# Optimization experiments

Hardware: AMD Instinct MI355X
Metric: run time of the kernel (lower is better)

## Reference

```python
import jax, jax.numpy as jnp
import numpy as np

N_GENE, N_CELL, N_GOTEM = 20000, 50000, 8000
D = 128
E_GC, E_GT = 600000, 200000


def _gconv(x_src, W, b, src, dst, n_src, n_dst):
    """DGL GraphConv with norm='both', bias, ReLU activation.
    out = relu(D_in^{-1/2} * scatter_sum_dst( (D_out^{-1/2} x_src) @ W ) + b)
    Degrees clamped to min 1, computed per edge type (as DGL does)."""
    ones = jnp.ones(src.shape[0], x_src.dtype)
    deg_out = jnp.clip(jax.ops.segment_sum(ones, src, num_segments=n_src), 1.0)
    deg_in = jnp.clip(jax.ops.segment_sum(ones, dst, num_segments=n_dst), 1.0)
    h = (x_src * (deg_out ** -0.5)[:, None]) @ W          # [n_src, d_out]
    agg = jax.ops.segment_sum(h[src], dst, num_segments=n_dst)  # gather + scatter-sum
    return jax.nn.relu(agg * (deg_in ** -0.5)[:, None] + b)


def setup_inputs() -> dict:
    key = jax.random.key(0)
    ks = iter(jax.random.split(key, 64))
    s = 1.0 / np.sqrt(D)
    inp = {
        "x_gene": jax.random.normal(next(ks), (N_GENE, D), jnp.float32),
        "x_cell": jax.random.normal(next(ks), (N_CELL, D), jnp.float32),
        "x_gotem": jax.random.normal(next(ks), (N_GOTEM, D), jnp.float32),
    }
    for name in ["W_eg_c2g", "W_eg_t2g", "W_eg_g2c", "W_et_g2t",
                 "W1_g2c", "W1_c2g", "W1_g2t", "W1_t2g",
                 "W2_g2c", "W2_c2g", "W2_g2t", "W2_t2g",
                 "W3_g2c", "Wd_cell"]:
        inp[name] = jax.random.normal(next(ks), (D, D), jnp.float32) * s
        inp[name.replace("W", "b", 1)] = jnp.zeros((D,), jnp.float32)
    inp["eg2c_src"] = jax.random.randint(next(ks), (E_GC,), 0, N_GENE, jnp.int32)
    inp["eg2c_dst"] = jax.random.randint(next(ks), (E_GC,), 0, N_CELL, jnp.int32)
    inp["ec2g_src"] = jax.random.randint(next(ks), (E_GC,), 0, N_CELL, jnp.int32)
    inp["ec2g_dst"] = jax.random.randint(next(ks), (E_GC,), 0, N_GENE, jnp.int32)
    inp["eg2t_src"] = jax.random.randint(next(ks), (E_GT,), 0, N_GENE, jnp.int32)
    inp["eg2t_dst"] = jax.random.randint(next(ks), (E_GT,), 0, N_GOTEM, jnp.int32)
    inp["et2g_src"] = jax.random.randint(next(ks), (E_GT,), 0, N_GOTEM, jnp.int32)
    inp["et2g_dst"] = jax.random.randint(next(ks), (E_GT,), 0, N_GENE, jnp.int32)
    return inp


def reference(x_gene, x_cell, x_gotem,
              W_eg_c2g, b_eg_c2g, W_eg_t2g, b_eg_t2g, W_eg_g2c, b_eg_g2c,
              W_et_g2t, b_et_g2t,
              W1_g2c, b1_g2c, W1_c2g, b1_c2g, W1_g2t, b1_g2t, W1_t2g, b1_t2g,
              W2_g2c, b2_g2c, W2_c2g, b2_c2g, W2_g2t, b2_g2t, W2_t2g, b2_t2g,
              W3_g2c, b3_g2c, Wd_cell, bd_cell,
              eg2c_src, eg2c_dst, ec2g_src, ec2g_dst,
              eg2t_src, eg2t_dst, et2g_src, et2g_dst):
    ng, nc, nt = x_gene.shape[0], x_cell.shape[0], x_gotem.shape[0]
    # embedding_gene: HeteroGraphConv(sum) -> gene gets cell2gene + gotem2gene, cell gets gene2cell
    h0_gene = (_gconv(x_cell, W_eg_c2g, b_eg_c2g, ec2g_src, ec2g_dst, nc, ng)
               + _gconv(x_gotem, W_eg_t2g, b_eg_t2g, et2g_src, et2g_dst, nt, ng))
    h0_cell = _gconv(x_gene, W_eg_g2c, b_eg_g2c, eg2c_src, eg2c_dst, ng, nc)
    g = jax.nn.relu(h0_gene)   # extra relu in forward (idempotent but faithful)
    c = jax.nn.relu(h0_cell)
    # embedding_gotem uses the UPDATED gene features
    t = _gconv(g, W_et_g2t, b_et_g2t, eg2t_src, eg2t_dst, ng, nt)
    # conv1
    g1 = (_gconv(c, W1_c2g, b1_c2g, ec2g_src, ec2g_dst, nc, ng)
          + _gconv(t, W1_t2g, b1_t2g, et2g_src, et2g_dst, nt, ng))
    c1 = _gconv(g, W1_g2c, b1_g2c, eg2c_src, eg2c_dst, ng, nc)
    t1 = _gconv(g, W1_g2t, b1_g2t, eg2t_src, eg2t_dst, ng, nt)
    # conv2
    g2 = (_gconv(c1, W2_c2g, b2_c2g, ec2g_src, ec2g_dst, nc, ng)
          + _gconv(t1, W2_t2g, b2_t2g, et2g_src, et2g_dst, nt, ng))
    c2 = _gconv(g1, W2_g2c, b2_g2c, eg2c_src, eg2c_dst, ng, nc)
    del t1
    # conv3: only the 'cell' output feeds the returned value
    c3 = _gconv(g2, W3_g2c, b3_g2c, eg2c_src, eg2c_dst, ng, nc)
    del c2
    # HeteroLinear on 'cell' (no activation)
    return c3 @ Wd_cell + bd_cell
```

## Files before the change

### kernel.cpp

```cpp
#include <hip/hip_runtime.h>
#include <hip/hip_fp16.h>

#define NG 20000
#define NC 50000
#define NT 8000
#define EGC 600000
#define EGT 200000
#define CHUNK 25000


struct HSeg { const int* idx; int* rep; int* pos; int ne, nb, bpr, nranges, nd; };
struct HTab { HSeg s[12]; };

static __global__ __launch_bounds__(1024)
void hist_lds_kernel(HTab tab) {
    __shared__ int h[12800];
    int b = blockIdx.x, sidx = 0;
    for (;;) {
        int nbl = tab.s[sidx].nb * tab.s[sidx].nranges;
        if (b < nbl) break;
        b -= nbl; ++sidx;
    }
    const HSeg g = tab.s[sidx];
    const int row = b % g.nb, range = b / g.nb;
    const int lo = range * g.bpr;
    const int hi = min(lo + g.bpr, g.nd);
    const int nbins = hi - lo;
    for (int i = threadIdx.x; i < nbins; i += 1024) h[i] = 0;
    __syncthreads();
    const int e0 = row * CHUNK;
    const int e1 = min(e0 + CHUNK, g.ne);
    if (g.pos) {
        for (int i = e0 + (int)threadIdx.x; i < e1; i += 1024) {
            int d = g.idx[i];
            if (d >= lo && d < hi) {
                int p = atomicAdd(&h[d - lo], 1);
                g.pos[i] = p;
            }
        }
    } else {
        for (int i = e0 + (int)threadIdx.x; i < e1; i += 1024) {
            int d = g.idx[i];
            if (d >= lo && d < hi) atomicAdd(&h[d - lo], 1);
        }
    }
    __syncthreads();
    int* rp = g.rep + (size_t)row * g.nd + lo;
    for (int i = threadIdx.x; i < nbins; i += 1024) rp[i] = h[i];
}


struct SPSeg { int* repd; const int* reps; float* so; float* si; int* ci_tot; int ns, nd, nb, len; };

static __device__ void sp_body(const SPSeg& s, int i) {
    if (i < s.ns) {
        int c = 0;
        for (int r = 0; r < s.nb; ++r) c += s.reps[(size_t)r * s.ns + i];
        if (c < 1) c = 1;
        s.so[i] = 1.0f / sqrtf((float)c);
    }
    if (i < s.nd) {
        int run = 0;
        for (int r = 0; r < s.nb; ++r) {
            int* p = s.repd + (size_t)r * s.nd + i;
            int t = *p; *p = run; run += t;
        }
        s.ci_tot[i] = run;
        int c = run < 1 ? 1 : run;
        s.si[i] = 1.0f / sqrtf((float)c);
    }
}

static __global__ __launch_bounds__(256)
void spscales4_kernel(SPSeg a, SPSeg b, SPSeg c, SPSeg d) {
    int i = blockIdx.x * 256 + threadIdx.x;
    if (i < a.len) { sp_body(a, i); return; }
    i -= a.len;
    if (i < b.len) { sp_body(b, i); return; }
    i -= b.len;
    if (i < c.len) { sp_body(c, i); return; }
    i -= c.len;
    if (i < d.len) { sp_body(d, i); }
}


static __global__ __launch_bounds__(256)
void xconv_kernel(const float* __restrict__ x, const float* __restrict__ so,
                  float2* __restrict__ out) {
    int i = blockIdx.x * 256 + threadIdx.x;
    if (i >= NC * 32) return;
    int row = i >> 5;
    float s = so[row];
    float4 v = reinterpret_cast<const float4*>(x)[i];
    float2 pk;
    *reinterpret_cast<__half2*>(&pk.x) = __floats2half2_rn(v.x * s, v.y * s);
    *reinterpret_cast<__half2*>(&pk.y) = __floats2half2_rn(v.z * s, v.w * s);
    out[i] = pk;
}


static __device__ void scan_body(const int* __restrict__ cnt, int* __restrict__ off, int n) {
    __shared__ int wsum[16];
    __shared__ int carry_s, total_s;
    const int t = threadIdx.x;
    const int lane = t & 63, wid = t >> 6;
    if (t == 0) carry_s = 0;
    __syncthreads();
    for (int base = 0; base < n; base += 8192) {
        int i0 = base + t * 8;
        int v[8];
        if (i0 + 8 <= n) {
            int4 a = *reinterpret_cast<const int4*>(cnt + i0);
            int4 b = *reinterpret_cast<const int4*>(cnt + i0 + 4);
            v[0]=a.x; v[1]=a.y; v[2]=a.z; v[3]=a.w; v[4]=b.x; v[5]=b.y; v[6]=b.z; v[7]=b.w;
        } else {
#pragma unroll
            for (int k = 0; k < 8; ++k) v[k] = (i0 + k < n) ? cnt[i0 + k] : 0;
        }
        int tsum = 0;
#pragma unroll
        for (int k = 0; k < 8; ++k) tsum += v[k];
        int x = tsum;
#pragma unroll
        for (int d = 1; d < 64; d <<= 1) {
            int y = __shfl_up(x, d, 64);
            if (lane >= d) x += y;
        }
        if (lane == 63) wsum[wid] = x;
        __syncthreads();
        if (wid == 0) {
            int w = (lane < 16) ? wsum[lane] : 0;
            int xx = w;
#pragma unroll
            for (int d = 1; d < 16; d <<= 1) {
                int y = __shfl_up(xx, d, 64);
                if (lane >= d) xx += y;
            }
            if (lane < 16) wsum[lane] = xx - w;
            if (lane == 15) total_s = xx;
        }
        __syncthreads();
        int run = carry_s + wsum[wid] + (x - tsum);
        if (i0 + 8 <= n) {
            int o[8];
#pragma unroll
            for (int k = 0; k < 8; ++k) { o[k] = run; run += v[k]; }
            *reinterpret_cast<int4*>(off + i0)     = make_int4(o[0], o[1], o[2], o[3]);
            *reinterpret_cast<int4*>(off + i0 + 4) = make_int4(o[4], o[5], o[6], o[7]);
        } else {
#pragma unroll
            for (int k = 0; k < 8; ++k) if (i0 + k < n) { off[i0 + k] = run; run += v[k]; }
        }
        __syncthreads();
        if (t == 0) carry_s += total_s;
        __syncthreads();
    }
    if (t == 0) off[n] = carry_s;
}

static __global__ __launch_bounds__(1024)
void scan4_kernel(const int* c0, int* o0, int n0,
                  const int* c1, int* o1, int n1,
                  const int* c2, int* o2, int n2,
                  const int* c3, int* o3, int n3) {
    if (blockIdx.x == 0) scan_body(c0, o0, n0);
    else if (blockIdx.x == 1) scan_body(c1, o1, n1);
    else if (blockIdx.x == 2) scan_body(c2, o2, n2);
    else scan_body(c3, o3, n3);
}


struct SSeg { const int* srce; const int* dste; const int* pos; const int* rep; const int* off; int* eid; int ne, nd; };

static __device__ void scatter_body(const SSeg& s, int i) {
    int row = i / CHUNK;
    int d = s.dste[i];
    s.eid[s.off[d] + s.rep[(size_t)row * s.nd + d] + s.pos[i]] = s.srce[i];
}

static __global__ __launch_bounds__(256)
void scatter4_kernel(SSeg a, SSeg b, SSeg c, SSeg d) {
    int i = blockIdx.x * 256 + threadIdx.x;
    if (i < a.ne) { scatter_body(a, i); return; }
    i -= a.ne;
    if (i < b.ne) { scatter_body(b, i); return; }
    i -= b.ne;
    if (i < c.ne) { scatter_body(c, i); return; }
    i -= c.ne;
    if (i < d.ne) { scatter_body(d, i); }
}


template<int RELU, int RH, int WH>
static __global__ __launch_bounds__(256)
void gemm_kernel(const void* __restrict__ Xv, const float* __restrict__ rs,
                 const float* __restrict__ W, const float* __restrict__ bias,
                 void* __restrict__ outv, int n) {
    __shared__ float xs[32][128];
    const int r0 = blockIdx.x * 32;
    const int t = threadIdx.x;
    for (int i = t; i < 1024; i += 256) {
        int r = i >> 5;
        int c4 = i & 31;
        int row = r0 + r;
        float4 v = make_float4(0.f, 0.f, 0.f, 0.f);
        if (row < n) {
            if (RH) {
                float2 pk = reinterpret_cast<const float2*>(Xv)[row * 32 + c4];
                float2 lo = __half22float2(*reinterpret_cast<__half2*>(&pk.x));
                float2 hi = __half22float2(*reinterpret_cast<__half2*>(&pk.y));
                v = make_float4(lo.x, lo.y, hi.x, hi.y);
            } else {
                v = reinterpret_cast<const float4*>(Xv)[row * 32 + c4];
            }
            if (rs) { float s = rs[row]; v.x *= s; v.y *= s; v.z *= s; v.w *= s; }
        }
        reinterpret_cast<float4*>(&xs[r][0])[c4] = v;
    }
    __syncthreads();
    const int tx = t & 31, ty = t >> 5;
    const int c0 = tx << 2;
    float acc[4][4] = {};
    const float* wp = W + c0;
    for (int k = 0; k < 128; k += 4) {
        float4 w0 = *reinterpret_cast<const float4*>(wp + (k + 0) * 128);
        float4 w1 = *reinterpret_cast<const float4*>(wp + (k + 1) * 128);
        float4 w2 = *reinterpret_cast<const float4*>(wp + (k + 2) * 128);
        float4 w3 = *reinterpret_cast<const float4*>(wp + (k + 3) * 128);
#pragma unroll
        for (int i = 0; i < 4; ++i) {
            float4 xv = *reinterpret_cast<const float4*>(&xs[ty * 4 + i][k]);
            acc[i][0] += xv.x * w0.x; acc[i][1] += xv.x * w0.y; acc[i][2] += xv.x * w0.z; acc[i][3] += xv.x * w0.w;
            acc[i][0] += xv.y * w1.x; acc[i][1] += xv.y * w1.y; acc[i][2] += xv.y * w1.z; acc[i][3] += xv.y * w1.w;
            acc[i][0] += xv.z * w2.x; acc[i][1] += xv.z * w2.y; acc[i][2] += xv.z * w2.z; acc[i][3] += xv.z * w2.w;
            acc[i][0] += xv.w * w3.x; acc[i][1] += xv.w * w3.y; acc[i][2] += xv.w * w3.z; acc[i][3] += xv.w * w3.w;
        }
    }
    float4 bv = make_float4(0.f, 0.f, 0.f, 0.f);
    if (bias) bv = reinterpret_cast<const float4*>(bias)[tx];
#pragma unroll
    for (int i = 0; i < 4; ++i) {
        int row = r0 + ty * 4 + i;
        if (row < n) {
            float4 o;
            o.x = acc[i][0] + bv.x; o.y = acc[i][1] + bv.y;
            o.z = acc[i][2] + bv.z; o.w = acc[i][3] + bv.w;
            if (RELU) {
                o.x = fmaxf(o.x, 0.f); o.y = fmaxf(o.y, 0.f);
                o.z = fmaxf(o.z, 0.f); o.w = fmaxf(o.w, 0.f);
            }
            if (WH) {
                float2 pk;
                *reinterpret_cast<__half2*>(&pk.x) = __floats2half2_rn(o.x, o.y);
                *reinterpret_cast<__half2*>(&pk.y) = __floats2half2_rn(o.z, o.w);
                reinterpret_cast<float2*>(outv)[row * 32 + tx] = pk;
            } else {
                reinterpret_cast<float4*>(outv)[row * 32 + tx] = o;
            }
        }
    }
}


template<int MODE, int OUTH>
static __global__ __launch_bounds__(256)
void agg_kernel(const __half2* __restrict__ h2, const float* __restrict__ pre,
                const int* __restrict__ off, const int* __restrict__ eid,
                const float* __restrict__ si, const float* __restrict__ bias,
                const float* __restrict__ post,
                void* __restrict__ outv, int n_dst) {
    int row = blockIdx.x * 4 + (threadIdx.x >> 6);
    if (row >= n_dst) return;
    int lane = threadIdx.x & 63;
    int e0 = off[row], e1 = off[row + 1];
    float ax = 0.f, ay = 0.f;
    int j = e0;
    for (; j + 8 <= e1; j += 8) {
        int s[8];
#pragma unroll
        for (int k = 0; k < 8; ++k) s[k] = eid[j + k];
        float2 f[8];
#pragma unroll
        for (int k = 0; k < 8; ++k) f[k] = __half22float2(h2[(size_t)s[k] * 64 + lane]);
        if (pre) {
#pragma unroll
            for (int k = 0; k < 8; ++k) { float p = pre[s[k]]; ax += f[k].x * p; ay += f[k].y * p; }
        } else {
#pragma unroll
            for (int k = 0; k < 8; ++k) { ax += f[k].x; ay += f[k].y; }
        }
    }
    for (; j < e1; ++j) {
        int s = eid[j];
        float2 f = __half22float2(h2[(size_t)s * 64 + lane]);
        float p = pre ? pre[s] : 1.0f;
        ax += f.x * p; ay += f.y * p;
    }
    int oidx = row * 64 + lane;
    if (MODE == 0) {
        reinterpret_cast<float2*>(outv)[oidx] = make_float2(ax, ay);
    } else {
        float s = si[row];
        float2 b = reinterpret_cast<const float2*>(bias)[lane];
        float ox = fmaxf(ax * s + b.x, 0.f);
        float oy = fmaxf(ay * s + b.y, 0.f);
        if (MODE == 1 && post) { float pm = post[row]; ox *= pm; oy *= pm; }
        if (OUTH) {
            __half2* o = reinterpret_cast<__half2*>(outv) + oidx;
            if (MODE == 2) { float2 cur = __half22float2(*o); ox += cur.x; oy += cur.y; }
            *o = __floats2half2_rn(ox, oy);
        } else {
            float2* o = reinterpret_cast<float2*>(outv) + oidx;
            if (MODE == 2) { float2 cur = *o; ox += cur.x; oy += cur.y; }
            *o = make_float2(ox, oy);
        }
    }
}


extern "C" void kernel_launch(void* const* d_in, const int* in_sizes, int n_in,
                              void* d_out, int out_size, void* d_ws, size_t ws_size,
                              hipStream_t stream) {
    const float* x_cell   = (const float*)d_in[1];
    const float* x_gotem  = (const float*)d_in[2];
    const float* W_eg_c2g = (const float*)d_in[3];  const float* b_eg_c2g = (const float*)d_in[4];
    const float* W_eg_t2g = (const float*)d_in[5];  const float* b_eg_t2g = (const float*)d_in[6];
    const float* W1_g2c   = (const float*)d_in[11]; const float* b1_g2c   = (const float*)d_in[12];
    const float* W1_g2t   = (const float*)d_in[15]; const float* b1_g2t   = (const float*)d_in[16];
    const float* W2_c2g   = (const float*)d_in[21]; const float* b2_c2g   = (const float*)d_in[22];
    const float* W2_t2g   = (const float*)d_in[25]; const float* b2_t2g   = (const float*)d_in[26];
    const float* W3_g2c   = (const float*)d_in[27]; const float* b3_g2c   = (const float*)d_in[28];
    const float* Wd_cell  = (const float*)d_in[29]; const float* bd_cell  = (const float*)d_in[30];
    const int* eg2c_src = (const int*)d_in[31]; const int* eg2c_dst = (const int*)d_in[32];
    const int* ec2g_src = (const int*)d_in[33]; const int* ec2g_dst = (const int*)d_in[34];
    const int* eg2t_src = (const int*)d_in[35]; const int* eg2t_dst = (const int*)d_in[36];
    const int* et2g_src = (const int*)d_in[37]; const int* et2g_dst = (const int*)d_in[38];

    char* p = (char*)d_ws;
    auto alloc = [&](size_t bytes) { char* r = p; p += (bytes + 255) & ~(size_t)255; return r; };
    float* h_buf = (float*)alloc((size_t)NC * 128 * 4);
    void*  g_buf = (void*)alloc((size_t)NG * 128 * 2);
    void*  c_buf = (void*)alloc((size_t)NC * 128 * 4);
    float* t_buf = (float*)alloc((size_t)NT * 128 * 4);
    void*  xch   = (void*)alloc((size_t)NC * 128 * 2);
    int* off_gc = (int*)alloc((NG + 1) * 4);  int* eid_gc = (int*)alloc((size_t)EGC * 4);
    int* off_gt = (int*)alloc((NG + 1) * 4);  int* eid_gt = (int*)alloc((size_t)EGT * 4);
    int* off_c  = (int*)alloc((NC + 1) * 4);  int* eid_c  = (int*)alloc((size_t)EGC * 4);
    int* off_t  = (int*)alloc((NT + 1) * 4);  int* eid_t  = (int*)alloc((size_t)EGT * 4);
    float* so_ec2g = (float*)alloc(NC * 4);
    float* so_et2g = (float*)alloc(NT * 4);
    float* so_eg2c = (float*)alloc(NG * 4);
    float* so_eg2t = (float*)alloc(NG * 4);
    float* si_ec2g = (float*)alloc(NG * 4);
    float* si_et2g = (float*)alloc(NG * 4);
    float* si_eg2c = (float*)alloc(NC * 4);
    float* si_eg2t = (float*)alloc(NT * 4);
    int* ct_a = (int*)alloc(NG * 4);
    int* ct_b = (int*)alloc(NG * 4);
    int* ct_c = (int*)alloc(NC * 4);
    int* ct_d = (int*)alloc(NT * 4);
    int* pos_a = (int*)alloc((size_t)EGC * 4);
    int* pos_b = (int*)alloc((size_t)EGT * 4);
    int* pos_c = (int*)alloc((size_t)EGC * 4);
    int* pos_d = (int*)alloc((size_t)EGT * 4);
    int* rd_a = (int*)alloc((size_t)24 * NG * 4);
    int* rd_b = (int*)alloc((size_t)8  * NG * 4);
    int* rd_c = (int*)alloc((size_t)24 * NC * 4);
    int* rd_d = (int*)alloc((size_t)8  * NT * 4);
    int* rs_a = (int*)alloc((size_t)24 * NC * 4);
    int* rs_b = (int*)alloc((size_t)8  * NT * 4);
    int* rs_c = (int*)alloc((size_t)24 * NG * 4);
    int* rs_d = (int*)alloc((size_t)8  * NG * 4);

    auto cdiv = [](int a, int b) { return (a + b - 1) / b; };
    const int ETOT = 2 * EGC + 2 * EGT;

    HTab tab;
    tab.s[0]  = {ec2g_dst, rd_a, pos_a, EGC, 24, 10000, 2, NG};
    tab.s[1]  = {et2g_dst, rd_b, pos_b, EGT,  8, 10000, 2, NG};
    tab.s[2]  = {eg2c_dst, rd_c, pos_c, EGC, 24, 12500, 4, NC};
    tab.s[3]  = {eg2t_dst, rd_d, pos_d, EGT,  8,  8000, 1, NT};
    tab.s[4]  = {ec2g_src, rs_a, nullptr, EGC, 24, 12500, 4, NC};
    tab.s[5]  = {et2g_src, rs_b, nullptr, EGT,  8,  8000, 1, NT};
    tab.s[6]  = {eg2c_src, rs_c, nullptr, EGC, 24, 10000, 2, NG};
    tab.s[7]  = {eg2t_src, rs_d, nullptr, EGT,  8, 10000, 2, NG};
    tab.s[8] = tab.s[9] = tab.s[10] = tab.s[11] = HSeg{nullptr, nullptr, nullptr, 0, 0, 1, 0, 0};
    int hist_blocks = 24*2 + 8*2 + 24*4 + 8*1 + 24*4 + 8*1 + 24*2 + 8*2;
    hist_lds_kernel<<<hist_blocks, 1024, 0, stream>>>(tab);

    SPSeg sa{rd_a, rs_a, so_ec2g, si_ec2g, ct_a, NC, NG, 24, NC};
    SPSeg sb{rd_b, rs_b, so_et2g, si_et2g, ct_b, NT, NG,  8, NG};
    SPSeg sc{rd_c, rs_c, so_eg2c, si_eg2c, ct_c, NG, NC, 24, NC};
    SPSeg sd{rd_d, rs_d, so_eg2t, si_eg2t, ct_d, NG, NT,  8, NG};
    spscales4_kernel<<<cdiv(NC + NG + NC + NG, 256), 256, 0, stream>>>(sa, sb, sc, sd);

    xconv_kernel<<<cdiv(NC * 32, 256), 256, 0, stream>>>(x_cell, so_ec2g, (float2*)xch);

    scan4_kernel<<<4, 1024, 0, stream>>>(ct_a, off_gc, NG, ct_b, off_gt, NG,
                                         ct_c, off_c, NC, ct_d, off_t, NT);

    SSeg ba{ec2g_src, ec2g_dst, pos_a, rd_a, off_gc, eid_gc, EGC, NG};
    SSeg bb{et2g_src, et2g_dst, pos_b, rd_b, off_gt, eid_gt, EGT, NG};
    SSeg bc{eg2c_src, eg2c_dst, pos_c, rd_c, off_c,  eid_c,  EGC, NC};
    SSeg bd{eg2t_src, eg2t_dst, pos_d, rd_d, off_t,  eid_t,  EGT, NT};
    scatter4_kernel<<<cdiv(ETOT, 256), 256, 0, stream>>>(ba, bb, bc, bd);

    agg_kernel<0,0><<<cdiv(NG, 4), 256, 0, stream>>>((const __half2*)xch, nullptr, off_gc, eid_gc, nullptr, nullptr, nullptr, h_buf, NG);
    gemm_kernel<1,0,1><<<cdiv(NG, 32), 256, 0, stream>>>(h_buf, si_ec2g, W_eg_c2g, b_eg_c2g, g_buf, NG);
    gemm_kernel<0,0,1><<<cdiv(NT, 32), 256, 0, stream>>>(x_gotem, so_et2g, W_eg_t2g, nullptr, h_buf, NT);
    agg_kernel<2,1><<<cdiv(NG, 4), 256, 0, stream>>>((const __half2*)h_buf, nullptr, off_gt, eid_gt, si_et2g, b_eg_t2g, nullptr, g_buf, NG);

    gemm_kernel<0,1,1><<<cdiv(NG, 32), 256, 0, stream>>>(g_buf, so_eg2c, W1_g2c, nullptr, h_buf, NG);
    agg_kernel<1,1><<<cdiv(NC, 4), 256, 0, stream>>>((const __half2*)h_buf, nullptr, off_c, eid_c, si_eg2c, b1_g2c, so_ec2g, c_buf, NC);

    agg_kernel<0,0><<<cdiv(NT, 4), 256, 0, stream>>>((const __half2*)g_buf, so_eg2t, off_t, eid_t, nullptr, nullptr, nullptr, h_buf, NT);
    gemm_kernel<1,0,0><<<cdiv(NT, 32), 256, 0, stream>>>(h_buf, si_eg2t, W1_g2t, b1_g2t, t_buf, NT);

    agg_kernel<0,0><<<cdiv(NG, 4), 256, 0, stream>>>((const __half2*)c_buf, nullptr, off_gc, eid_gc, nullptr, nullptr, nullptr, h_buf, NG);
    gemm_kernel<1,0,1><<<cdiv(NG, 32), 256, 0, stream>>>(h_buf, si_ec2g, W2_c2g, b2_c2g, g_buf, NG);
    gemm_kernel<0,0,1><<<cdiv(NT, 32), 256, 0, stream>>>(t_buf, so_et2g, W2_t2g, nullptr, h_buf, NT);
    agg_kernel<2,1><<<cdiv(NG, 4), 256, 0, stream>>>((const __half2*)h_buf, nullptr, off_gt, eid_gt, si_et2g, b2_t2g, nullptr, g_buf, NG);

    gemm_kernel<0,1,1><<<cdiv(NG, 32), 256, 0, stream>>>(g_buf, so_eg2c, W3_g2c, nullptr, h_buf, NG);
    agg_kernel<1,0><<<cdiv(NC, 4), 256, 0, stream>>>((const __half2*)h_buf, nullptr, off_c, eid_c, si_eg2c, b3_g2c, nullptr, c_buf, NC);

    gemm_kernel<0,0,0><<<cdiv(NC, 32), 256, 0, stream>>>(c_buf, nullptr, Wd_cell, bd_cell, d_out, NC);
}
```

Measured before the change: 566.8 us.

## Replace FP32 SIMT GEMMs with fp16 MFMA GEMMs and keep all intermediates in half

Adds a kernel that converts the eight 128x128 weight matrices into an fp16 MFMA-friendly layout. All dense transforms now run through a new MFMA 16x16x32 fp16 GEMM that applies the per-row scale after the product. Every intermediate buffer (aggregation outputs, t, c) is stored in fp16 instead of fp32, which cuts memory traffic in the aggregation and GEMM stages. The cost is an extra pack kernel and an extra conversion of x_gotem, plus reduced precision in more places.

```diff
diff --git a/kernel.cpp b/kernel.cpp
--- a/kernel.cpp
+++ b/kernel.cpp
@@ -7,6 +7,9 @@
 #define EGC 600000
 #define EGT 200000
 #define CHUNK 25000
+
+typedef _Float16 h8 __attribute__((ext_vector_type(8)));
+typedef float f4 __attribute__((ext_vector_type(4)));
 
 
 struct HSeg { const int* idx; int* rep; int* pos; int ne, nb, bpr, nranges, nd; };
@@ -86,16 +89,34 @@
 
 static __global__ __launch_bounds__(256)
 void xconv_kernel(const float* __restrict__ x, const float* __restrict__ so,
-                  float2* __restrict__ out) {
+                  float2* __restrict__ out, int ngran) {
     int i = blockIdx.x * 256 + threadIdx.x;
-    if (i >= NC * 32) return;
+    if (i >= ngran) return;
     int row = i >> 5;
-    float s = so[row];
+    float s = so ? so[row] : 1.0f;
     float4 v = reinterpret_cast<const float4*>(x)[i];
     float2 pk;
     *reinterpret_cast<__half2*>(&pk.x) = __floats2half2_rn(v.x * s, v.y * s);
     *reinterpret_cast<__half2*>(&pk.y) = __floats2half2_rn(v.z * s, v.w * s);
     out[i] = pk;
+}
+
+
+struct PackTab { const float* w[8]; };
+
+static __global__ __launch_bounds__(256)
+void pack_kernel(PackTab pt, _Float16* __restrict__ wp) {
+    int wi = blockIdx.x >> 3;
+    int t = ((blockIdx.x & 7) << 8) + threadIdx.x;
+    int lane = t & 63, kk = (t >> 6) & 3, ct = t >> 8;
+    int g = lane >> 4, r = lane & 15;
+    const float* W = pt.w[wi];
+    int n = ct * 16 + r;
+    int kbase = kk * 32 + g * 8;
+    h8 v;
+#pragma unroll
+    for (int j = 0; j < 8; ++j) v[j] = (_Float16)W[(kbase + j) * 128 + n];
+    *reinterpret_cast<h8*>(wp + (size_t)wi * 16384 + (size_t)t * 8) = v;
 }
 
 
@@ -191,84 +212,62 @@
 }
 
 
-template<int RELU, int RH, int WH>
-static __global__ __launch_bounds__(256)
-void gemm_kernel(const void* __restrict__ Xv, const float* __restrict__ rs,
-                 const float* __restrict__ W, const float* __restrict__ bias,
-                 void* __restrict__ outv, int n) {
-    __shared__ float xs[32][128];
-    const int r0 = blockIdx.x * 32;
-    const int t = threadIdx.x;
-    for (int i = t; i < 1024; i += 256) {
-        int r = i >> 5;
-        int c4 = i & 31;
-        int row = r0 + r;
-        float4 v = make_float4(0.f, 0.f, 0.f, 0.f);
-        if (row < n) {
-            if (RH) {
-                float2 pk = reinterpret_cast<const float2*>(Xv)[row * 32 + c4];
-                float2 lo = __half22float2(*reinterpret_cast<__half2*>(&pk.x));
-                float2 hi = __half22float2(*reinterpret_cast<__half2*>(&pk.y));
-                v = make_float4(lo.x, lo.y, hi.x, hi.y);
-            } else {
-                v = reinterpret_cast<const float4*>(Xv)[row * 32 + c4];
+template<int RELU, int WH>
+static __global__ __launch_bounds__(256)
+void gemm_mfma(const _Float16* __restrict__ X, const float* __restrict__ scale,
+               const _Float16* __restrict__ Wp, const float* __restrict__ bias,
+               void* __restrict__ outv, int n) {
+    const int wave = threadIdx.x >> 6, lane = threadIdx.x & 63;
+    const int g = lane >> 4, r = lane & 15;
+    const int r0 = blockIdx.x * 64 + wave * 16;
+    const int arow = r0 + r;
+    h8 a[4];
+    if (arow < n) {
+        const _Float16* xr = X + (size_t)arow * 128;
+#pragma unroll
+        for (int kk = 0; kk < 4; ++kk)
+            a[kk] = *reinterpret_cast<const h8*>(xr + kk * 32 + g * 8);
+    } else {
+#pragma unroll
+        for (int kk = 0; kk < 4; ++kk)
+#pragma unroll
+            for (int j = 0; j < 8; ++j) a[kk][j] = (_Float16)0.f;
+    }
+    int orow[4]; float sc[4];
+#pragma unroll
+    for (int reg = 0; reg < 4; ++reg) {
+        orow[reg] = r0 + g * 4 + reg;
+        sc[reg] = (scale && orow[reg] < n) ? scale[orow[reg]] : 1.0f;
+    }
+    const h8* bp = reinterpret_cast<const h8*>(Wp);
+#pragma unroll
+    for (int ct = 0; ct < 8; ++ct) {
+        f4 acc = {0.f, 0.f, 0.f, 0.f};
+#pragma unroll
+        for (int kk = 0; kk < 4; ++kk)
+            acc = __builtin_amdgcn_mfma_f32_16x16x32_f16(a[kk], bp[(ct * 4 + kk) * 64 + lane], acc, 0, 0, 0);
+        float bx = bias ? bias[ct * 16 + r] : 0.f;
+#pragma unroll
+        for (int reg = 0; reg < 4; ++reg) {
+            int row = orow[reg];
+            if (row < n) {
+                float o = acc[reg] * sc[reg] + bx;
+                if (RELU) o = fmaxf(o, 0.f);
+                if (WH) reinterpret_cast<_Float16*>(outv)[(size_t)row * 128 + ct * 16 + r] = (_Float16)o;
+                else    reinterpret_cast<float*>(outv)[(size_t)row * 128 + ct * 16 + r] = o;
             }
-            if (rs) { float s = rs[row]; v.x *= s; v.y *= s; v.z *= s; v.w *= s; }
-        }
-        reinterpret_cast<float4*>(&xs[r][0])[c4] = v;
-    }
-    __syncthreads();
-    const int tx = t & 31, ty = t >> 5;
-    const int c0 = tx << 2;
-    float acc[4][4] = {};
-    const float* wp = W + c0;
-    for (int k = 0; k < 128; k += 4) {
-        float4 w0 = *reinterpret_cast<const float4*>(wp + (k + 0) * 128);
-        float4 w1 = *reinterpret_cast<const float4*>(wp + (k + 1) * 128);
-        float4 w2 = *reinterpret_cast<const float4*>(wp + (k + 2) * 128);
-        float4 w3 = *reinterpret_cast<const float4*>(wp + (k + 3) * 128);
-#pragma unroll
-        for (int i = 0; i < 4; ++i) {
-            float4 xv = *reinterpret_cast<const float4*>(&xs[ty * 4 + i][k]);
-            acc[i][0] += xv.x * w0.x; acc[i][1] += xv.x * w0.y; acc[i][2] += xv.x * w0.z; acc[i][3] += xv.x * w0.w;
-            acc[i][0] += xv.y * w1.x; acc[i][1] += xv.y * w1.y; acc[i][2] += xv.y * w1.z; acc[i][3] += xv.y * w1.w;
-            acc[i][0] += xv.z * w2.x; acc[i][1] += xv.z * w2.y; acc[i][2] += xv.z * w2.z; acc[i][3] += xv.z * w2.w;
-            acc[i][0] += xv.w * w3.x; acc[i][1] += xv.w * w3.y; acc[i][2] += xv.w * w3.z; acc[i][3] += xv.w * w3.w;
-        }
-    }
-    float4 bv = make_float4(0.f, 0.f, 0.f, 0.f);
-    if (bias) bv = reinterpret_cast<const float4*>(bias)[tx];
-#pragma unroll
-    for (int i = 0; i < 4; ++i) {
-        int row = r0 + ty * 4 + i;
-        if (row < n) {
-            float4 o;
-            o.x = acc[i][0] + bv.x; o.y = acc[i][1] + bv.y;
-            o.z = acc[i][2] + bv.z; o.w = acc[i][3] + bv.w;
-            if (RELU) {
-                o.x = fmaxf(o.x, 0.f); o.y = fmaxf(o.y, 0.f);
-                o.z = fmaxf(o.z, 0.f); o.w = fmaxf(o.w, 0.f);
-            }
-            if (WH) {
-                float2 pk;
-                *reinterpret_cast<__half2*>(&pk.x) = __floats2half2_rn(o.x, o.y);
-                *reinterpret_cast<__half2*>(&pk.y) = __floats2half2_rn(o.z, o.w);
-                reinterpret_cast<float2*>(outv)[row * 32 + tx] = pk;
-            } else {
-                reinterpret_cast<float4*>(outv)[row * 32 + tx] = o;
-            }
-        }
-    }
-}
-
-
-template<int MODE, int OUTH>
+        }
+    }
+}
+
+
+template<int MODE>
 static __global__ __launch_bounds__(256)
 void agg_kernel(const __half2* __restrict__ h2, const float* __restrict__ pre,
                 const int* __restrict__ off, const int* __restrict__ eid,
                 const float* __restrict__ si, const float* __restrict__ bias,
                 const float* __restrict__ post,
-                void* __restrict__ outv, int n_dst) {
+                __half2* __restrict__ out, int n_dst) {
     int row = blockIdx.x * 4 + (threadIdx.x >> 6);
     if (row >= n_dst) return;
     int lane = threadIdx.x & 63;
@@ -296,24 +295,17 @@
         float p = pre ? pre[s] : 1.0f;
         ax += f.x * p; ay += f.y * p;
     }
-    int oidx = row * 64 + lane;
+    __half2* o = out + (size_t)row * 64 + lane;
     if (MODE == 0) {
-        reinterpret_cast<float2*>(outv)[oidx] = make_float2(ax, ay);
+        *o = __floats2half2_rn(ax, ay);
     } else {
         float s = si[row];
         float2 b = reinterpret_cast<const float2*>(bias)[lane];
         float ox = fmaxf(ax * s + b.x, 0.f);
         float oy = fmaxf(ay * s + b.y, 0.f);
         if (MODE == 1 && post) { float pm = post[row]; ox *= pm; oy *= pm; }
-        if (OUTH) {
-            __half2* o = reinterpret_cast<__half2*>(outv) + oidx;
-            if (MODE == 2) { float2 cur = __half22float2(*o); ox += cur.x; oy += cur.y; }
-            *o = __floats2half2_rn(ox, oy);
-        } else {
-            float2* o = reinterpret_cast<float2*>(outv) + oidx;
-            if (MODE == 2) { float2 cur = *o; ox += cur.x; oy += cur.y; }
-            *o = make_float2(ox, oy);
-        }
+        if (MODE == 2) { float2 cur = __half22float2(*o); ox += cur.x; oy += cur.y; }
+        *o = __floats2half2_rn(ox, oy);
     }
 }
 
@@ -338,11 +330,13 @@
 
     char* p = (char*)d_ws;
     auto alloc = [&](size_t bytes) { char* r = p; p += (bytes + 255) & ~(size_t)255; return r; };
-    float* h_buf = (float*)alloc((size_t)NC * 128 * 4);
-    void*  g_buf = (void*)alloc((size_t)NG * 128 * 2);
-    void*  c_buf = (void*)alloc((size_t)NC * 128 * 4);
-    float* t_buf = (float*)alloc((size_t)NT * 128 * 4);
-    void*  xch   = (void*)alloc((size_t)NC * 128 * 2);
+    _Float16* h16 = (_Float16*)alloc((size_t)NG * 128 * 2);
+    _Float16* g16 = (_Float16*)alloc((size_t)NG * 128 * 2);
+    _Float16* c16 = (_Float16*)alloc((size_t)NC * 128 * 2);
+    _Float16* t16 = (_Float16*)alloc((size_t)NT * 128 * 2);
+    _Float16* xch = (_Float16*)alloc((size_t)NC * 128 * 2);
+    _Float16* xgh = (_Float16*)alloc((size_t)NT * 128 * 2);
+    _Float16* wpk = (_Float16*)alloc((size_t)8 * 16384 * 2);
     int* off_gc = (int*)alloc((NG + 1) * 4);  int* eid_gc = (int*)alloc((size_t)EGC * 4);
     int* off_gt = (int*)alloc((NG + 1) * 4);  int* eid_gt = (int*)alloc((size_t)EGT * 4);
     int* off_c  = (int*)alloc((NC + 1) * 4);  int* eid_c  = (int*)alloc((size_t)EGC * 4);
@@ -375,6 +369,15 @@
     auto cdiv = [](int a, int b) { return (a + b - 1) / b; };
     const int ETOT = 2 * EGC + 2 * EGT;
 
+    PackTab pt;
+    pt.w[0] = W_eg_c2g; pt.w[1] = W_eg_t2g; pt.w[2] = W1_g2c; pt.w[3] = W1_g2t;
+    pt.w[4] = W2_c2g;   pt.w[5] = W2_t2g;   pt.w[6] = W3_g2c; pt.w[7] = Wd_cell;
+    pack_kernel<<<64, 256, 0, stream>>>(pt, wpk);
+    _Float16* Wp_egc = wpk + 0 * 16384; _Float16* Wp_egt = wpk + 1 * 16384;
+    _Float16* Wp_1gc = wpk + 2 * 16384; _Float16* Wp_1gt = wpk + 3 * 16384;
+    _Float16* Wp_2cg = wpk + 4 * 16384; _Float16* Wp_2tg = wpk + 5 * 16384;
+    _Float16* Wp_3gc = wpk + 6 * 16384; _Float16* Wp_d   = wpk + 7 * 16384;
+
     HTab tab;
     tab.s[0]  = {ec2g_dst, rd_a, pos_a, EGC, 24, 10000, 2, NG};
     tab.s[1]  = {et2g_dst, rd_b, pos_b, EGT,  8, 10000, 2, NG};
@@ -394,7 +397,8 @@
     SPSeg sd{rd_d, rs_d, so_eg2t, si_eg2t, ct_d, NG, NT,  8, NG};
     spscales4_kernel<<<cdiv(NC + NG + NC + NG, 256), 256, 0, stream>>>(sa, sb, sc, sd);
 
-    xconv_kernel<<<cdiv(NC * 32, 256), 256, 0, stream>>>(x_cell, so_ec2g, (float2*)xch);
+    xconv_kernel<<<cdiv(NC * 32, 256), 256, 0, stream>>>(x_cell, so_ec2g, (float2*)xch, NC * 32);
+    xconv_kernel<<<cdiv(NT * 32, 256), 256, 0, stream>>>(x_gotem, nullptr, (float2*)xgh, NT * 32);
 
     scan4_kernel<<<4, 1024, 0, stream>>>(ct_a, off_gc, NG, ct_b, off_gt, NG,
                                          ct_c, off_c, NC, ct_d, off_t, NT);
@@ -405,24 +409,24 @@
     SSeg bd{eg2t_src, eg2t_dst, pos_d, rd_d, off_t,  eid_t,  EGT, NT};
     scatter4_kernel<<<cdiv(ETOT, 256), 256, 0, stream>>>(ba, bb, bc, bd);
 
-    agg_kernel<0,0><<<cdiv(NG, 4), 256, 0, stream>>>((const __half2*)xch, nullptr, off_gc, eid_gc, nullptr, nullptr, nullptr, h_buf, NG);
-    gemm_kernel<1,0,1><<<cdiv(NG, 32), 256, 0, stream>>>(h_buf, si_ec2g, W_eg_c2g, b_eg_c2g, g_buf, NG);
-    gemm_kernel<0,0,1><<<cdiv(NT, 32), 256, 0, stream>>>(x_gotem, so_et2g, W_eg_t2g, nullptr, h_buf, NT);
-    agg_kernel<2,1><<<cdiv(NG, 4), 256, 0, stream>>>((const __half2*)h_buf, nullptr, off_gt, eid_gt, si_et2g, b_eg_t2g, nullptr, g_buf, NG);
-
-    gemm_kernel<0,1,1><<<cdiv(NG, 32), 256, 0, stream>>>(g_buf, so_eg2c, W1_g2c, nullptr, h_buf, NG);
-    agg_kernel<1,1><<<cdiv(NC, 4), 256, 0, stream>>>((const __half2*)h_buf, nullptr, off_c, eid_c, si_eg2c, b1_g2c, so_ec2g, c_buf, NC);
-
-    agg_kernel<0,0><<<cdiv(NT, 4), 256, 0, stream>>>((const __half2*)g_buf, so_eg2t, off_t, eid_t, nullptr, nullptr, nullptr, h_buf, NT);
-    gemm_kernel<1,0,0><<<cdiv(NT, 32), 256, 0, stream>>>(h_buf, si_eg2t, W1_g2t, b1_g2t, t_buf, NT);
-
-    agg_kernel<0,0><<<cdiv(NG, 4), 256, 0, stream>>>((const __half2*)c_buf, nullptr, off_gc, eid_gc, nullptr, nullptr, nullptr, h_buf, NG);
-    gemm_kernel<1,0,1><<<cdiv(NG, 32), 256, 0, stream>>>(h_buf, si_ec2g, W2_c2g, b2_c2g, g_buf, NG);
-    gemm_kernel<0,0,1><<<cdiv(NT, 32), 256, 0, stream>>>(t_buf, so_et2g, W2_t2g, nullptr, h_buf, NT);
-    agg_kernel<2,1><<<cdiv(NG, 4), 256, 0, stream>>>((const __half2*)h_buf, nullptr, off_gt, eid_gt, si_et2g, b2_t2g, nullptr, g_buf, NG);
-
-    gemm_kernel<0,1,1><<<cdiv(NG, 32), 256, 0, stream>>>(g_buf, so_eg2c, W3_g2c, nullptr, h_buf, NG);
-    agg_kernel<1,0><<<cdiv(NC, 4), 256, 0, stream>>>((const __half2*)h_buf, nullptr, off_c, eid_c, si_eg2c, b3_g2c, nullptr, c_buf, NC);
-
-    gemm_kernel<0,0,0><<<cdiv(NC, 32), 256, 0, stream>>>(c_buf, nullptr, Wd_cell, bd_cell, d_out, NC);
-}
+    agg_kernel<0><<<cdiv(NG, 4), 256, 0, stream>>>((const __half2*)xch, nullptr, off_gc, eid_gc, nullptr, nullptr, nullptr, (__half2*)h16, NG);
+    gemm_mfma<1,1><<<cdiv(NG, 64), 256, 0, stream>>>(h16, si_ec2g, Wp_egc, b_eg_c2g, g16, NG);
+    gemm_mfma<0,1><<<cdiv(NT, 64), 256, 0, stream>>>(xgh, so_et2g, Wp_egt, nullptr, h16, NT);
+    agg_kernel<2><<<cdiv(NG, 4), 256, 0, stream>>>((const __half2*)h16, nullptr, off_gt, eid_gt, si_et2g, b_eg_t2g, nullptr, (__half2*)g16, NG);
+
+    gemm_mfma<0,1><<<cdiv(NG, 64), 256, 0, stream>>>(g16, so_eg2c, Wp_1gc, nullptr, h16, NG);
+    agg_kernel<1><<<cdiv(NC, 4), 256, 0, stream>>>((const __half2*)h16, nullptr, off_c, eid_c, si_eg2c, b1_g2c, so_ec2g, (__half2*)c16, NC);
+
+    agg_kernel<0><<<cdiv(NT, 4), 256, 0, stream>>>((const __half2*)g16, so_eg2t, off_t, eid_t, nullptr, nullptr, nullptr, (__half2*)h16, NT);
+    gemm_mfma<1,1><<<cdiv(NT, 64), 256, 0, stream>>>(h16, si_eg2t, Wp_1gt, b1_g2t, t16, NT);
+
+    agg_kernel<0><<<cdiv(NG, 4), 256, 0, stream>>>((const __half2*)c16, nullptr, off_gc, eid_gc, nullptr, nullptr, nullptr, (__half2*)h16, NG);
+    gemm_mfma<1,1><<<cdiv(NG, 64), 256, 0, stream>>>(h16, si_ec2g, Wp_2cg, b2_c2g, g16, NG);
+    gemm_mfma<0,1><<<cdiv(NT, 64), 256, 0, stream>>>(t16, so_et2g, Wp_2tg, nullptr, h16, NT);
+    agg_kernel<2><<<cdiv(NG, 4), 256, 0, stream>>>((const __half2*)h16, nullptr, off_gt, eid_gt, si_et2g, b2_t2g, nullptr, (__half2*)g16, NG);
+
+    gemm_mfma<0,1><<<cdiv(NG, 64), 256, 0, stream>>>(g16, so_eg2c, Wp_3gc, nullptr, h16, NG);
+    agg_kernel<1><<<cdiv(NC, 4), 256, 0, stream>>>((const __half2*)h16, nullptr, off_c, eid_c, si_eg2c, b3_g2c, nullptr, (__half2*)c16, NC);
+
+    gemm_mfma<0,0><<<cdiv(NC, 64), 256, 0, stream>>>(c16, nullptr, Wp_d, bd_cell, d_out, NC);
+}
```

Measured after the change: 492.9 us. 13.0% less time.
